# Performance work log

Measured on AMD Instinct MI355X. Metric: run time of the kernel, lower is better.

The kernel has to match this reference:

```python
import jax, jax.numpy as jnp
import numpy as np

MIN_SI = 0.01
MAX_SI = 1.0


def setup_inputs() -> dict:
    key = jax.random.key(0)
    ks = jax.random.split(key, 6)
    B, T, D, U = 256, 512, 1024, 1024
    inputs = jax.random.normal(ks[0], (B, T, D), dtype=jnp.float32)
    h0 = jnp.zeros((B, U), dtype=jnp.float32)
    kernel = jax.random.normal(ks[1], (D, U), dtype=jnp.float32) * (1.0 / np.sqrt(D))
    recurrent_kernel = jax.random.normal(ks[2], (U, U), dtype=jnp.float32) * (1.0 / np.sqrt(U))
    bias = jnp.zeros((U,), dtype=jnp.float32)
    # 'spread' mu init + sigma=0.1 as in mu_si_initializer
    mu_current = jnp.asarray(np.linspace(0.2, 0.8, U), dtype=jnp.float32)
    sigma_current = jnp.full((U,), 0.1, dtype=jnp.float32)
    mu_prev = jnp.asarray(np.linspace(0.2, 0.8, U), dtype=jnp.float32)
    sigma_prev = jnp.full((U,), 0.1, dtype=jnp.float32)
    return {
        "inputs": inputs, "h0": h0, "kernel": kernel,
        "recurrent_kernel": recurrent_kernel, "bias": bias,
        "mu_current": mu_current, "sigma_current": sigma_current,
        "mu_prev": mu_prev, "sigma_prev": sigma_prev,
    }


def _calc_U(idxs, mu, sigma, input_dim):
    # idxs: [n_in], mu/sigma: [units] -> returns [n_in, units]
    up = (idxs[None, :] - mu[:, None]) ** 2            # [units, n_in]
    s = jnp.clip(sigma, MIN_SI, MAX_SI)
    dwn = (2.0 * s * s)[:, None]
    res = jnp.exp(-up / dwn)
    # normed == 2: l2-normalize rows then scale by sqrt(input_dim)
    res = res / jnp.sqrt(jnp.sum(res * res, axis=-1, keepdims=True))
    res = res * jnp.sqrt(jnp.float32(input_dim))
    return res.T


def reference(inputs, h0, kernel, recurrent_kernel, bias,
              mu_current, sigma_current, mu_prev, sigma_prev):
    D, U = kernel.shape
    idxs_current = jnp.asarray(np.linspace(0.0, 1.0, D), dtype=jnp.float32)
    idxs_prev = jnp.asarray(np.linspace(0.0, 1.0, U), dtype=jnp.float32)
    # Focus masks (identical every timestep, so computed once)
    u_current = _calc_U(idxs_current, mu_current, sigma_current, D)   # [D, U]
    u_previous = _calc_U(idxs_prev, mu_prev, sigma_prev, D)           # [U, U] (note: sqrt(input_dim) per source)
    kernel_current = kernel * u_current
    kernel_previous = recurrent_kernel * u_previous

    def step(h, x_t):
        # x_t: [B, D], h: [B, U]
        h_new = jnp.tanh(x_t @ kernel_current + bias + h @ kernel_previous)
        return h_new, h_new

    xs = jnp.swapaxes(inputs, 0, 1)  # [T, B, D]
    _, ys = jax.lax.scan(step, h0, xs)
    return jnp.swapaxes(ys, 0, 1)    # [B, T, U]
```

## Files before the change

kernel.cpp:

```cpp
#include <hip/hip_runtime.h>
#include <cmath>

#define BN 256
#define TN 512
#define DN 1024
#define UN 1024
#define STEPS_P1 (TN + 1)

typedef _Float16 half8 __attribute__((ext_vector_type(8)));
typedef _Float16 half4v __attribute__((ext_vector_type(4)));
typedef float floatx4 __attribute__((ext_vector_type(4)));

__global__ __launch_bounds__(256) void prep_weights(
    const float* __restrict__ kernel,
    const float* __restrict__ rkernel,
    const float* __restrict__ mu_c, const float* __restrict__ si_c,
    const float* __restrict__ mu_p, const float* __restrict__ si_p,
    _Float16* __restrict__ WcT,
    _Float16* __restrict__ WpT)
{
    __shared__ float g[1024];
    __shared__ float red[256];
    const int j = blockIdx.x;
    const bool prev = (blockIdx.y == 1);
    const float* K = prev ? rkernel : kernel;
    float mu = prev ? mu_p[j] : mu_c[j];
    float si = prev ? si_p[j] : si_c[j];
    si = fminf(fmaxf(si, 0.01f), 1.0f);
    const float inv2s2 = 1.0f / (2.0f * si * si);
    const float step = 1.0f / 1023.0f;

    float ss = 0.0f;
#pragma unroll
    for (int s = 0; s < 4; ++s) {
        int i = threadIdx.x + s * 256;
        float d = (float)i * step - mu;
        float v = expf(-d * d * inv2s2);
        g[i] = v;
        ss += v * v;
    }
    red[threadIdx.x] = ss;
    __syncthreads();
    for (int off = 128; off > 0; off >>= 1) {
        if (threadIdx.x < (unsigned)off) red[threadIdx.x] += red[threadIdx.x + off];
        __syncthreads();
    }
    const float scale = 32.0f * rsqrtf(red[0]);
    _Float16* dst = prev ? WpT : WcT;
#pragma unroll
    for (int s = 0; s < 4; ++s) {
        int i = threadIdx.x + s * 256;
        dst[(long)j * 1024 + i] = (_Float16)(K[(long)i * 1024 + j] * g[i] * scale);
    }
}

__global__ __launch_bounds__(512, 2) void gemm_z(
    const float* __restrict__ X,
    const _Float16* __restrict__ WcT,
    const float* __restrict__ bias,
    float* __restrict__ Z)
{
    __shared__ _Float16 lA[64 * 40];

    const int tid  = threadIdx.x;
    const int wave = tid >> 6;
    const int lane = tid & 63;
    const int q    = lane >> 4;
    const int ln   = lane & 15;
    const int ncol0 = wave * 128;
    const long m_base = (long)blockIdx.x * 64;

    const int arow = tid >> 3;
    const int acq  = tid & 7;

    floatx4 acc[4][8];
#pragma unroll
    for (int ms = 0; ms < 4; ++ms)
#pragma unroll
        for (int ns = 0; ns < 8; ++ns) acc[ms][ns] = (floatx4){0.f, 0.f, 0.f, 0.f};

    for (int k0 = 0; k0 < 1024; k0 += 32) {
        float4 v = *(const float4*)(X + (m_base + arow) * 1024 + k0 + acq * 4);
        half4v hv = { (_Float16)v.x, (_Float16)v.y, (_Float16)v.z, (_Float16)v.w };
        *(half4v*)(&lA[arow * 40 + acq * 4]) = hv;
        __syncthreads();

        half8 a[4];
#pragma unroll
        for (int ms = 0; ms < 4; ++ms)
            a[ms] = *(const half8*)(&lA[(ms * 16 + ln) * 40 + q * 8]);

#pragma unroll
        for (int ns = 0; ns < 8; ++ns) {
            half8 b = *(const half8*)(WcT + (long)(ncol0 + ns * 16 + ln) * 1024 + k0 + q * 8);
#pragma unroll
            for (int ms = 0; ms < 4; ++ms)
                acc[ms][ns] = __builtin_amdgcn_mfma_f32_16x16x32_f16(a[ms], b, acc[ms][ns], 0, 0, 0);
        }
        __syncthreads();
    }

#pragma unroll
    for (int ns = 0; ns < 8; ++ns) {
        int col = ncol0 + ns * 16 + ln;
        float bs = bias[col];
#pragma unroll
        for (int ms = 0; ms < 4; ++ms) {
#pragma unroll
            for (int r = 0; r < 4; ++r) {
                long row = m_base + ms * 16 + q * 4 + r;
                Z[row * 1024 + col] = acc[ms][ns][r] + bs;
            }
        }
    }
}

__device__ __forceinline__ float fast_tanh(float x) {
    return 1.0f - 2.0f / (__expf(2.0f * x) + 1.0f);
}

__global__ __launch_bounds__(256, 1) void rnn_scan(
    const _Float16* __restrict__ WpT,
    float* __restrict__ Zout,
    _Float16* __restrict__ hbuf,
    unsigned* __restrict__ cnt)
{
    __shared__ _Float16 hs[16 * 1032];

    const int tid  = threadIdx.x;
    const int wave = tid >> 6;
    const int lane = tid & 63;
    const int q    = lane >> 4;
    const int ln   = lane & 15;
    const int bi   = blockIdx.x >> 4;
    const int nj   = blockIdx.x & 15;
    const int ncol0 = nj * 64 + wave * 16;
    const int hrow  = bi * 16 + ln;

    unsigned* mycnt = cnt + bi * STEPS_P1;

    half8 b[32];
    {
        const _Float16* bp = WpT + (long)(ncol0 + ln) * 1024 + q * 8;
#pragma unroll
        for (int kk = 0; kk < 32; ++kk) b[kk] = *(const half8*)(bp + kk * 32);
    }

    {
        unsigned long long* p = (unsigned long long*)
            (hbuf + (long)(bi * 16 + (tid >> 4)) * 1024 + nj * 64 + (tid & 15) * 4);
        __hip_atomic_store(p, 0ull, __ATOMIC_RELAXED, __HIP_MEMORY_SCOPE_AGENT);
    }
    asm volatile("s_waitcnt vmcnt(0)" ::: "memory");
    __syncthreads();
    if (tid == 0)
        __hip_atomic_fetch_add(&mycnt[0], 1u, __ATOMIC_RELAXED, __HIP_MEMORY_SCOPE_AGENT);

    for (int t = 0; t < TN; ++t) {
        const long zoff = ((long)hrow * TN + t) * 1024 + ncol0 + q * 4;
        float4 z = *(const float4*)(Zout + zoff);

        if (tid == 0) {
            while (__hip_atomic_load(&mycnt[t], __ATOMIC_RELAXED, __HIP_MEMORY_SCOPE_AGENT) < 16u)
                __builtin_amdgcn_s_sleep(1);
        }
        __syncthreads();
        __builtin_amdgcn_fence(__ATOMIC_ACQUIRE, "workgroup");

        const unsigned long long* hp = (const unsigned long long*)
            (hbuf + (long)(t & 1) * (BN * UN) + (long)bi * 16 * 1024);
        unsigned long long tmp[16];
#pragma unroll
        for (int i = 0; i < 16; ++i)
            tmp[i] = __hip_atomic_load(hp + i * 256 + tid, __ATOMIC_RELAXED, __HIP_MEMORY_SCOPE_AGENT);
#pragma unroll
        for (int i = 0; i < 16; ++i) {
            int d   = i * 256 + tid;
            int row = d >> 8;
            int c8  = d & 255;
            *(unsigned long long*)(hs + row * 1032 + c8 * 4) = tmp[i];
        }
        __syncthreads();

        floatx4 acc[4];
#pragma unroll
        for (int c4 = 0; c4 < 4; ++c4) acc[c4] = (floatx4){0.f, 0.f, 0.f, 0.f};
#pragma unroll
        for (int kk = 0; kk < 32; ++kk) {
            half8 a = *(const half8*)(hs + ln * 1032 + kk * 32 + q * 8);
            acc[kk & 3] = __builtin_amdgcn_mfma_f32_16x16x32_f16(b[kk], a, acc[kk & 3], 0, 0, 0);
        }
        floatx4 s = (acc[0] + acc[1]) + (acc[2] + acc[3]);

        float4 hv;
        hv.x = fast_tanh(z.x + s[0]);
        hv.y = fast_tanh(z.y + s[1]);
        hv.z = fast_tanh(z.z + s[2]);
        hv.w = fast_tanh(z.w + s[3]);
        *(float4*)(Zout + zoff) = hv;

        union { _Float16 h[4]; unsigned long long u; } pk;
        pk.h[0] = (_Float16)hv.x; pk.h[1] = (_Float16)hv.y;
        pk.h[2] = (_Float16)hv.z; pk.h[3] = (_Float16)hv.w;
        unsigned long long* hn = (unsigned long long*)
            (hbuf + (long)((t + 1) & 1) * (BN * UN) + (long)hrow * 1024 + ncol0 + q * 4);
        __hip_atomic_store(hn, pk.u, __ATOMIC_RELAXED, __HIP_MEMORY_SCOPE_AGENT);

        asm volatile("s_waitcnt vmcnt(0)" ::: "memory");
        __syncthreads();
        if (tid == 0)
            __hip_atomic_fetch_add(&mycnt[t + 1], 1u, __ATOMIC_RELAXED, __HIP_MEMORY_SCOPE_AGENT);
    }
}

extern "C" void kernel_launch(void* const* d_in, const int* in_sizes, int n_in,
                              void* d_out, int out_size, void* d_ws, size_t ws_size,
                              hipStream_t stream) {
    (void)in_sizes; (void)n_in; (void)out_size; (void)ws_size;
    const float* X    = (const float*)d_in[0];
    const float* K    = (const float*)d_in[2];
    const float* RK   = (const float*)d_in[3];
    const float* bias = (const float*)d_in[4];
    const float* muc  = (const float*)d_in[5];
    const float* sic  = (const float*)d_in[6];
    const float* mup  = (const float*)d_in[7];
    const float* sip  = (const float*)d_in[8];
    float* out = (float*)d_out;

    _Float16* WcT  = (_Float16*)d_ws;
    _Float16* WpT  = WcT + 1024 * 1024;
    _Float16* hbuf = (_Float16*)d_ws;
    unsigned* cnt  = (unsigned*)((char*)d_ws + (1u << 20));

    prep_weights<<<dim3(1024, 2), 256, 0, stream>>>(K, RK, muc, sic, mup, sip, WcT, WpT);
    gemm_z<<<dim3((BN * TN) / 64), 512, 0, stream>>>(X, WcT, bias, out);

    hipMemsetAsync(cnt, 0, 16 * STEPS_P1 * sizeof(unsigned), stream);

    const _Float16* WpT_c = WpT;
    float* out_p = out;
    _Float16* hbuf_p = hbuf;
    unsigned* cnt_p = cnt;
    void* kargs[] = { (void*)&WpT_c, (void*)&out_p, (void*)&hbuf_p, (void*)&cnt_p };
    hipLaunchCooperativeKernel((const void*)rnn_scan, dim3(16 * 16), dim3(256),
                               kargs, 0, stream);
}
```

Measured before the change: 3.200 ms.

## Retile input GEMM to 256x256 blocks with prefetch and swizzled LDS

The input-projection GEMM now uses 1024-thread blocks computing 256x256 output tiles with a K-step of 64. X is register-prefetched for the next step and stored to an XOR-swizzled LDS layout instead of a padded one. The RNN scan kernel also switches its hidden-state LDS tile to an XOR swizzle, and moves the fp32 output store after the counter signal so it leaves the inter-block critical path. The aim is more reuse of X and weights per block, fewer LDS bank conflicts, and a shorter per-step latency, at the cost of higher register pressure and lower occupancy in the GEMM.

```diff
diff --git a/kernel.cpp b/kernel.cpp
--- a/kernel.cpp
+++ b/kernel.cpp
@@ -54,61 +54,85 @@
     }
 }
 
-__global__ __launch_bounds__(512, 2) void gemm_z(
+__global__ __launch_bounds__(1024) void gemm_z(
     const float* __restrict__ X,
     const _Float16* __restrict__ WcT,
     const float* __restrict__ bias,
     float* __restrict__ Z)
 {
-    __shared__ _Float16 lA[64 * 40];
+    __shared__ _Float16 lA[256 * 64];
 
     const int tid  = threadIdx.x;
     const int wave = tid >> 6;
     const int lane = tid & 63;
     const int q    = lane >> 4;
     const int ln   = lane & 15;
-    const int ncol0 = wave * 128;
-    const long m_base = (long)blockIdx.x * 64;
-
-    const int arow = tid >> 3;
-    const int acq  = tid & 7;
-
-    floatx4 acc[4][8];
+    const int wr   = wave >> 2;
+    const int wc   = wave & 3;
+    const long m_base = (long)(blockIdx.x >> 2) * 256;
+    const int  c_base = (blockIdx.x & 3) * 256 + wc * 64;
+
+    const int srow  = tid >> 4;
+    const int sk    = (tid & 15) * 4;
+    const int swz_w = (srow & 7) << 4;
+    const int swz_r = (ln & 7) << 4;
+
+    floatx4 acc[4][4];
 #pragma unroll
     for (int ms = 0; ms < 4; ++ms)
 #pragma unroll
-        for (int ns = 0; ns < 8; ++ns) acc[ms][ns] = (floatx4){0.f, 0.f, 0.f, 0.f};
-
-    for (int k0 = 0; k0 < 1024; k0 += 32) {
-        float4 v = *(const float4*)(X + (m_base + arow) * 1024 + k0 + acq * 4);
-        half4v hv = { (_Float16)v.x, (_Float16)v.y, (_Float16)v.z, (_Float16)v.w };
-        *(half4v*)(&lA[arow * 40 + acq * 4]) = hv;
-        __syncthreads();
-
-        half8 a[4];
-#pragma unroll
-        for (int ms = 0; ms < 4; ++ms)
-            a[ms] = *(const half8*)(&lA[(ms * 16 + ln) * 40 + q * 8]);
-
-#pragma unroll
-        for (int ns = 0; ns < 8; ++ns) {
-            half8 b = *(const half8*)(WcT + (long)(ncol0 + ns * 16 + ln) * 1024 + k0 + q * 8);
-#pragma unroll
-            for (int ms = 0; ms < 4; ++ms)
-                acc[ms][ns] = __builtin_amdgcn_mfma_f32_16x16x32_f16(a[ms], b, acc[ms][ns], 0, 0, 0);
-        }
-        __syncthreads();
-    }
-
-#pragma unroll
-    for (int ns = 0; ns < 8; ++ns) {
-        int col = ncol0 + ns * 16 + ln;
+        for (int ns = 0; ns < 4; ++ns) acc[ms][ns] = (floatx4){0.f, 0.f, 0.f, 0.f};
+
+    float4 pf[4];
+#pragma unroll
+    for (int p = 0; p < 4; ++p)
+        pf[p] = *(const float4*)(X + (m_base + srow + p * 64) * 1024 + sk);
+
+    for (int k0 = 0; k0 < 1024; k0 += 64) {
+#pragma unroll
+        for (int p = 0; p < 4; ++p) {
+            int r = srow + p * 64;
+            half4v hv = { (_Float16)pf[p].x, (_Float16)pf[p].y,
+                          (_Float16)pf[p].z, (_Float16)pf[p].w };
+            *(half4v*)(&lA[r * 64 + (((sk * 2) ^ swz_w) >> 1)]) = hv;
+        }
+        __syncthreads();
+
+        if (k0 < 960) {
+#pragma unroll
+            for (int p = 0; p < 4; ++p)
+                pf[p] = *(const float4*)(X + (m_base + srow + p * 64) * 1024 + k0 + 64 + sk);
+        }
+
+#pragma unroll
+        for (int kk = 0; kk < 2; ++kk) {
+            half8 a[4];
+#pragma unroll
+            for (int ms = 0; ms < 4; ++ms) {
+                int row = wr * 64 + ms * 16 + ln;
+                a[ms] = *(const half8*)(&lA[row * 64 + (((kk * 64 + q * 16) ^ swz_r) >> 1)]);
+            }
+#pragma unroll
+            for (int ns = 0; ns < 4; ++ns) {
+                half8 b = *(const half8*)(WcT + (long)(c_base + ns * 16 + ln) * 1024
+                                              + k0 + kk * 32 + q * 8);
+#pragma unroll
+                for (int ms = 0; ms < 4; ++ms)
+                    acc[ms][ns] = __builtin_amdgcn_mfma_f32_16x16x32_f16(a[ms], b, acc[ms][ns], 0, 0, 0);
+            }
+        }
+        __syncthreads();
+    }
+
+#pragma unroll
+    for (int ns = 0; ns < 4; ++ns) {
+        int col = c_base + ns * 16 + ln;
         float bs = bias[col];
 #pragma unroll
         for (int ms = 0; ms < 4; ++ms) {
 #pragma unroll
             for (int r = 0; r < 4; ++r) {
-                long row = m_base + ms * 16 + q * 4 + r;
+                long row = m_base + wr * 64 + ms * 16 + q * 4 + r;
                 Z[row * 1024 + col] = acc[ms][ns][r] + bs;
             }
         }
@@ -125,7 +149,7 @@
     _Float16* __restrict__ hbuf,
     unsigned* __restrict__ cnt)
 {
-    __shared__ _Float16 hs[16 * 1032];
+    __shared__ _Float16 hs[16 * 1024];
 
     const int tid  = threadIdx.x;
     const int wave = tid >> 6;
@@ -136,6 +160,7 @@
     const int nj   = blockIdx.x & 15;
     const int ncol0 = nj * 64 + wave * 16;
     const int hrow  = bi * 16 + ln;
+    const int swz_r = (ln & 7) << 4;
 
     unsigned* mycnt = cnt + bi * STEPS_P1;
 
@@ -175,10 +200,8 @@
             tmp[i] = __hip_atomic_load(hp + i * 256 + tid, __ATOMIC_RELAXED, __HIP_MEMORY_SCOPE_AGENT);
 #pragma unroll
         for (int i = 0; i < 16; ++i) {
-            int d   = i * 256 + tid;
-            int row = d >> 8;
-            int c8  = d & 255;
-            *(unsigned long long*)(hs + row * 1032 + c8 * 4) = tmp[i];
+            int byte = (tid * 8) ^ ((i & 7) << 4);
+            *(unsigned long long*)(hs + i * 1024 + (byte >> 1)) = tmp[i];
         }
         __syncthreads();
 
@@ -187,7 +210,7 @@
         for (int c4 = 0; c4 < 4; ++c4) acc[c4] = (floatx4){0.f, 0.f, 0.f, 0.f};
 #pragma unroll
         for (int kk = 0; kk < 32; ++kk) {
-            half8 a = *(const half8*)(hs + ln * 1032 + kk * 32 + q * 8);
+            half8 a = *(const half8*)(hs + ln * 1024 + (((kk * 64 + q * 16) ^ swz_r) >> 1));
             acc[kk & 3] = __builtin_amdgcn_mfma_f32_16x16x32_f16(b[kk], a, acc[kk & 3], 0, 0, 0);
         }
         floatx4 s = (acc[0] + acc[1]) + (acc[2] + acc[3]);
@@ -197,7 +220,6 @@
         hv.y = fast_tanh(z.y + s[1]);
         hv.z = fast_tanh(z.z + s[2]);
         hv.w = fast_tanh(z.w + s[3]);
-        *(float4*)(Zout + zoff) = hv;
 
         union { _Float16 h[4]; unsigned long long u; } pk;
         pk.h[0] = (_Float16)hv.x; pk.h[1] = (_Float16)hv.y;
@@ -210,6 +232,8 @@
         __syncthreads();
         if (tid == 0)
             __hip_atomic_fetch_add(&mycnt[t + 1], 1u, __ATOMIC_RELAXED, __HIP_MEMORY_SCOPE_AGENT);
+
+        *(float4*)(Zout + zoff) = hv;
     }
 }
 
@@ -233,7 +257,7 @@
     unsigned* cnt  = (unsigned*)((char*)d_ws + (1u << 20));
 
     prep_weights<<<dim3(1024, 2), 256, 0, stream>>>(K, RK, muc, sic, mup, sip, WcT, WpT);
-    gemm_z<<<dim3((BN * TN) / 64), 512, 0, stream>>>(X, WcT, bias, out);
+    gemm_z<<<dim3((BN * TN / 256) * 4), 1024, 0, stream>>>(X, WcT, bias, out);
 
     hipMemsetAsync(cnt, 0, 16 * STEPS_P1 * sizeof(unsigned), stream);
 
```

Result: faster. 3.084 ms (-3.6%).
